# Kernel optimization log

Hardware: AMD Instinct MI355X
Metric: run time of the kernel (lower is better)

## Reference

```python
import jax, jax.numpy as jnp
import numpy as np
from jax.scipy.ndimage import map_coordinates

GRID_SIZE = 8
SIGMA = 0.05


def setup_inputs() -> dict:
    key = jax.random.key(0)
    k1, k2 = jax.random.split(key)
    B, C, D, H, W = 4, 2, 160, 160, 160
    x = jax.random.normal(k1, (B, C, D, H, W), dtype=jnp.float32)
    # torch.randn(B,3,g,g,g)*sigma hoisted out of forward for determinism
    flow_coarse = jax.random.normal(k2, (B, 3, GRID_SIZE, GRID_SIZE, GRID_SIZE), dtype=jnp.float32) * SIGMA
    return {"x": x, "flow_coarse": flow_coarse}


def _upsample_trilinear(f, D, H, W):
    # f: [g,g,g] coarse flow channel -> [D,H,W]; matches
    # F.interpolate(mode='trilinear', align_corners=True):
    # src coordinate = dst * (g-1)/(size-1), linear interp.
    g = f.shape[0]
    cz = jnp.arange(D, dtype=jnp.float32) * (g - 1) / (D - 1)
    cy = jnp.arange(H, dtype=jnp.float32) * (g - 1) / (H - 1)
    cx = jnp.arange(W, dtype=jnp.float32) * (g - 1) / (W - 1)
    mz, my, mx = jnp.meshgrid(cz, cy, cx, indexing='ij')
    return map_coordinates(f, [mz, my, mx], order=1, mode='nearest')


def reference(x, flow_coarse):
    B, C, D, H, W = x.shape
    # upsample coarse flow per (batch, channel): [B,3,D,H,W]
    up = jax.vmap(jax.vmap(lambda f: _upsample_trilinear(f, D, H, W)))(flow_coarse)
    # base normalized grid, channels ordered (x=w, y=h, z=d) as in grid_sample
    d = jnp.linspace(-1.0, 1.0, D, dtype=jnp.float32)
    h = jnp.linspace(-1.0, 1.0, H, dtype=jnp.float32)
    w = jnp.linspace(-1.0, 1.0, W, dtype=jnp.float32)
    gd, gh, gw = jnp.meshgrid(d, h, w, indexing='ij')
    gx = gw[None] + up[:, 0]  # [B,D,H,W]
    gy = gh[None] + up[:, 1]
    gz = gd[None] + up[:, 2]
    # unnormalize (align_corners=True): [-1,1] -> [0, size-1]
    ix = (gx + 1.0) * (W - 1) * 0.5
    iy = (gy + 1.0) * (H - 1) * 0.5
    iz = (gz + 1.0) * (D - 1) * 0.5

    # grid_sample 3D, bilinear(=trilinear), padding_mode='reflection',
    # align_corners=True == map_coordinates mode='mirror' (period 2*(n-1))
    def warp_bc(vol, cz, cy, cx):
        return map_coordinates(vol, [cz, cy, cx], order=1, mode='mirror')

    warp_b = jax.vmap(warp_bc, in_axes=(0, None, None, None))  # over C
    out = jax.vmap(warp_b)(x, iz, iy, ix)  # over B -> [B,C,D,H,W]
    return out
```

## Files before the change

### kernel.cpp

```cpp
#include <hip/hip_runtime.h>

#define NB 4
#define NC 2
#define ND 160
#define NH 160
#define NW 160
#define NG 8
#define HWSZ (NH * NW)
#define DHW (ND * HWSZ)
#define NTHR 256
#define NBLOCKS (NB * DHW / NTHR)
#define BLK_PER_B (DHW / NTHR)
#define BLK_PER_D (HWSZ / NTHR)
#define TILES_X 10
#define TILES_PER_SLICE 400

typedef float v2f __attribute__((ext_vector_type(2), aligned(4)));

__device__ __forceinline__ float reflect_mirror(float t) {
    t = fabsf(t);
    return fminf(t, 318.0f - t);
}

__device__ __forceinline__ float lerp_v(v2f q, float g) {
    return q.x + (q.y - q.x) * g;
}

__global__ __launch_bounds__(256) void elastic_deform_kernel(
    const float* __restrict__ x,
    const float* __restrict__ flow,
    float* __restrict__ out)
{
    int bid = blockIdx.x;
    int eff = (bid & 7) * (NBLOCKS / 8) + (bid >> 3);

    int b  = eff / BLK_PER_B;
    int e2 = eff - b * BLK_PER_B;
    int d  = e2 / BLK_PER_D;
    int e3 = e2 - d * BLK_PER_D;

    int wid  = (int)threadIdx.x >> 6;
    int lane = (int)threadIdx.x & 63;
    int tslice = e3 * 4 + wid;
    int ty = tslice / TILES_X;
    int tx = tslice - ty * TILES_X;
    int h  = ty * 4 + (lane >> 4);
    int w  = tx * 16 + (lane & 15);

    const float s = 7.0f / 159.0f;

    float cz  = (float)d * s;
    int   izb = min((int)cz, NG - 2);
    float fz  = cz - (float)izb;

    __shared__ float sfz[3 * 64];
    if (threadIdx.x < 192) {
        int ch = (int)threadIdx.x >> 6;
        int yx = (int)threadIdx.x & 63;
        const float* fp = flow + ((b * 3 + ch) * NG + izb) * 64 + yx;
        float f0 = fp[0], f1 = fp[64];
        sfz[ch * 64 + yx] = f0 + (f1 - f0) * fz;
    }
    __syncthreads();

    float cy = (float)h * s;
    float cx = (float)w * s;
    int iyb = min((int)cy, NG - 2); float fy = cy - (float)iyb;
    int ixb = min((int)cx, NG - 2); float fx = cx - (float)ixb;
    int cpos = iyb * NG + ixb;

    float u[3];
#pragma unroll
    for (int ch = 0; ch < 3; ++ch) {
        const float* p = sfz + ch * 64 + cpos;
        float f00 = p[0], f01 = p[1], f10 = p[8], f11 = p[9];
        float a0 = f00 + (f01 - f00) * fx;
        float a1 = f10 + (f11 - f10) * fx;
        u[ch] = a0 + (a1 - a0) * fy;
    }

    float sx = reflect_mirror((float)w + u[0] * 79.5f);
    float sy = reflect_mirror((float)h + u[1] * 79.5f);
    float sz = reflect_mirror((float)d + u[2] * 79.5f);

    int xb = min((int)sx, NW - 2); float gx = sx - (float)xb;
    int yb = min((int)sy, NH - 2); float gy = sy - (float)yb;
    int zb = min((int)sz, ND - 2); float gz = sz - (float)zb;

    int off = (zb * NH + yb) * NW + xb;
    const float* p0 = x + (size_t)b * (NC * DHW) + off;
    const float* p1 = p0 + DHW;

    float r0, r1;
    {
        float v00 = lerp_v(*(const v2f*)(p0), gx);
        float v01 = lerp_v(*(const v2f*)(p0 + NW), gx);
        float v10 = lerp_v(*(const v2f*)(p0 + HWSZ), gx);
        float v11 = lerp_v(*(const v2f*)(p0 + HWSZ + NW), gx);
        float a0 = v00 + (v01 - v00) * gy;
        float a1 = v10 + (v11 - v10) * gy;
        r0 = a0 + (a1 - a0) * gz;
    }
    {
        float v00 = lerp_v(*(const v2f*)(p1), gx);
        float v01 = lerp_v(*(const v2f*)(p1 + NW), gx);
        float v10 = lerp_v(*(const v2f*)(p1 + HWSZ), gx);
        float v11 = lerp_v(*(const v2f*)(p1 + HWSZ + NW), gx);
        float a0 = v00 + (v01 - v00) * gy;
        float a1 = v10 + (v11 - v10) * gy;
        r1 = a0 + (a1 - a0) * gz;
    }

    size_t opos = (size_t)b * (NC * DHW) + (size_t)(d * NH + h) * NW + w;
    __builtin_nontemporal_store(r0, out + opos);
    __builtin_nontemporal_store(r1, out + opos + DHW);
}

extern "C" void kernel_launch(void* const* d_in, const int* in_sizes, int n_in,
                              void* d_out, int out_size, void* d_ws, size_t ws_size,
                              hipStream_t stream) {
    const float* x    = (const float*)d_in[0];
    const float* flow = (const float*)d_in[1];
    float* out = (float*)d_out;
    elastic_deform_kernel<<<NBLOCKS, NTHR, 0, stream>>>(x, flow, out);
}
```

Baseline: 342.4 us.

## Compute two adjacent x outputs per thread with shared 4-wide gathers

Each thread now produces two neighbouring w outputs, loading one 4-float window per row that covers both samples and evaluating the x interpolation as a piecewise-linear blend. When the second sample lands in a different row or slice or outside the window, it falls back to separate 2-float loads. Coarse flow values are shared between the two outputs, and the stores become 2-wide. This halves the thread count and reduces the number of gather instructions, at the cost of more arithmetic, more registers and a divergent fallback path.

Measured after the change: 364.7 us. 1.06x slower.

```diff
diff --git a/kernel.cpp b/kernel.cpp
--- a/kernel.cpp
+++ b/kernel.cpp
@@ -9,21 +9,22 @@
 #define HWSZ (NH * NW)
 #define DHW (ND * HWSZ)
 #define NTHR 256
-#define NBLOCKS (NB * DHW / NTHR)
-#define BLK_PER_B (DHW / NTHR)
-#define BLK_PER_D (HWSZ / NTHR)
-#define TILES_X 10
-#define TILES_PER_SLICE 400
+#define NBLOCKS 32000
+#define BLK_PER_B 8000
+#define BLK_PER_D 50
+#define TILES_X 5
 
 typedef float v2f __attribute__((ext_vector_type(2), aligned(4)));
+typedef float v4fa __attribute__((ext_vector_type(4), aligned(4)));
 
 __device__ __forceinline__ float reflect_mirror(float t) {
     t = fabsf(t);
     return fminf(t, 318.0f - t);
 }
 
-__device__ __forceinline__ float lerp_v(v2f q, float g) {
-    return q.x + (q.y - q.x) * g;
+__device__ __forceinline__ float lerp2(const float* __restrict__ p, float g) {
+    float a = p[0], b = p[1];
+    return a + (b - a) * g;
 }
 
 __global__ __launch_bounds__(256) void elastic_deform_kernel(
@@ -45,7 +46,7 @@
     int ty = tslice / TILES_X;
     int tx = tslice - ty * TILES_X;
     int h  = ty * 4 + (lane >> 4);
-    int w  = tx * 16 + (lane & 15);
+    int w0 = tx * 32 + (lane & 15) * 2;
 
     const float s = 7.0f / 159.0f;
 
@@ -64,56 +65,122 @@
     __syncthreads();
 
     float cy = (float)h * s;
-    float cx = (float)w * s;
     int iyb = min((int)cy, NG - 2); float fy = cy - (float)iyb;
-    int ixb = min((int)cx, NG - 2); float fx = cx - (float)ixb;
-    int cpos = iyb * NG + ixb;
-
-    float u[3];
+    float cx0 = (float)w0 * s;
+    int ixa = min((int)cx0, NG - 2);
+    float e[3][3];
 #pragma unroll
     for (int ch = 0; ch < 3; ++ch) {
-        const float* p = sfz + ch * 64 + cpos;
-        float f00 = p[0], f01 = p[1], f10 = p[8], f11 = p[9];
-        float a0 = f00 + (f01 - f00) * fx;
-        float a1 = f10 + (f11 - f10) * fx;
-        u[ch] = a0 + (a1 - a0) * fy;
+        const float* p = sfz + ch * 64 + iyb * NG;
+#pragma unroll
+        for (int j = 0; j < 3; ++j) {
+            int ix = (j == 2) ? min(ixa + 2, NG - 1) : (ixa + j);
+            float f0 = p[ix], f1 = p[NG + ix];
+            e[ch][j] = f0 + (f1 - f0) * fy;
+        }
     }
 
-    float sx = reflect_mirror((float)w + u[0] * 79.5f);
-    float sy = reflect_mirror((float)h + u[1] * 79.5f);
-    float sz = reflect_mirror((float)d + u[2] * 79.5f);
+    int xb[2], yb[2], zb[2];
+    float sxv[2], gy[2], gz[2];
+#pragma unroll
+    for (int i = 0; i < 2; ++i) {
+        float cx = cx0 + (float)i * s;
+        int ixb = min((int)cx, NG - 2);
+        int oi  = ixb - ixa;
+        float fx = cx - (float)ixb;
+        float s0, s1;
+        s0 = oi ? e[0][1] : e[0][0];  s1 = oi ? e[0][2] : e[0][1];
+        float ux = s0 + (s1 - s0) * fx;
+        s0 = oi ? e[1][1] : e[1][0];  s1 = oi ? e[1][2] : e[1][1];
+        float uy = s0 + (s1 - s0) * fx;
+        s0 = oi ? e[2][1] : e[2][0];  s1 = oi ? e[2][2] : e[2][1];
+        float uz = s0 + (s1 - s0) * fx;
 
-    int xb = min((int)sx, NW - 2); float gx = sx - (float)xb;
-    int yb = min((int)sy, NH - 2); float gy = sy - (float)yb;
-    int zb = min((int)sz, ND - 2); float gz = sz - (float)zb;
+        float sx = reflect_mirror((float)(w0 + i) + ux * 79.5f);
+        float sy = reflect_mirror((float)h + uy * 79.5f);
+        float sz = reflect_mirror((float)d + uz * 79.5f);
+        xb[i] = min((int)sx, NW - 2); sxv[i] = sx;
+        yb[i] = min((int)sy, NH - 2); gy[i] = sy - (float)yb[i];
+        zb[i] = min((int)sz, ND - 2); gz[i] = sz - (float)zb[i];
+    }
 
-    int off = (zb * NH + yb) * NW + xb;
-    const float* p0 = x + (size_t)b * (NC * DHW) + off;
+    int xq = min(xb[0], NW - 4);
+    const float* basep = x + (size_t)b * (NC * DHW);
+    const float* p0 = basep + (zb[0] * NH + yb[0]) * NW + xq;
     const float* p1 = p0 + DHW;
 
-    float r0, r1;
+    v4fa qa0 = *(const v4fa*)(p0);
+    v4fa qa1 = *(const v4fa*)(p0 + NW);
+    v4fa qa2 = *(const v4fa*)(p0 + HWSZ);
+    v4fa qa3 = *(const v4fa*)(p0 + HWSZ + NW);
+    v4fa qb0 = *(const v4fa*)(p1);
+    v4fa qb1 = *(const v4fa*)(p1 + NW);
+    v4fa qb2 = *(const v4fa*)(p1 + HWSZ);
+    v4fa qb3 = *(const v4fa*)(p1 + HWSZ + NW);
+
+    float posA = sxv[0] - (float)xq;
+    float A1 = fminf(posA, 1.0f);
+    float A2 = fminf(fmaxf(posA - 1.0f, 0.0f), 1.0f);
+    float A3 = fminf(fmaxf(posA - 2.0f, 0.0f), 1.0f);
+    float posB = sxv[1] - (float)xq;
+    float B1 = fminf(posB, 1.0f);
+    float B2 = fminf(fmaxf(posB - 1.0f, 0.0f), 1.0f);
+    float B3 = fminf(fmaxf(posB - 2.0f, 0.0f), 1.0f);
+
+#define PWL(q, m1, m2, m3) \
+    ((q).x + (m1) * ((q).y - (q).x) + (m2) * ((q).z - (q).y) + (m3) * ((q).w - (q).z))
+
+    float r0c0, r0c1;
     {
-        float v00 = lerp_v(*(const v2f*)(p0), gx);
-        float v01 = lerp_v(*(const v2f*)(p0 + NW), gx);
-        float v10 = lerp_v(*(const v2f*)(p0 + HWSZ), gx);
-        float v11 = lerp_v(*(const v2f*)(p0 + HWSZ + NW), gx);
-        float a0 = v00 + (v01 - v00) * gy;
-        float a1 = v10 + (v11 - v10) * gy;
-        r0 = a0 + (a1 - a0) * gz;
-    }
-    {
-        float v00 = lerp_v(*(const v2f*)(p1), gx);
-        float v01 = lerp_v(*(const v2f*)(p1 + NW), gx);
-        float v10 = lerp_v(*(const v2f*)(p1 + HWSZ), gx);
-        float v11 = lerp_v(*(const v2f*)(p1 + HWSZ + NW), gx);
-        float a0 = v00 + (v01 - v00) * gy;
-        float a1 = v10 + (v11 - v10) * gy;
-        r1 = a0 + (a1 - a0) * gz;
+        float a0 = PWL(qa0, A1, A2, A3) + (PWL(qa1, A1, A2, A3) - PWL(qa0, A1, A2, A3)) * gy[0];
+        float a1 = PWL(qa2, A1, A2, A3) + (PWL(qa3, A1, A2, A3) - PWL(qa2, A1, A2, A3)) * gy[0];
+        r0c0 = a0 + (a1 - a0) * gz[0];
+        float b0 = PWL(qb0, A1, A2, A3) + (PWL(qb1, A1, A2, A3) - PWL(qb0, A1, A2, A3)) * gy[0];
+        float b1 = PWL(qb2, A1, A2, A3) + (PWL(qb3, A1, A2, A3) - PWL(qb2, A1, A2, A3)) * gy[0];
+        r0c1 = b0 + (b1 - b0) * gz[0];
     }
 
-    size_t opos = (size_t)b * (NC * DHW) + (size_t)(d * NH + h) * NW + w;
-    __builtin_nontemporal_store(r0, out + opos);
-    __builtin_nontemporal_store(r1, out + opos + DHW);
+    float r1c0, r1c1;
+    {
+        float a0 = PWL(qa0, B1, B2, B3) + (PWL(qa1, B1, B2, B3) - PWL(qa0, B1, B2, B3)) * gy[1];
+        float a1 = PWL(qa2, B1, B2, B3) + (PWL(qa3, B1, B2, B3) - PWL(qa2, B1, B2, B3)) * gy[1];
+        r1c0 = a0 + (a1 - a0) * gz[1];
+        float b0 = PWL(qb0, B1, B2, B3) + (PWL(qb1, B1, B2, B3) - PWL(qb0, B1, B2, B3)) * gy[1];
+        float b1 = PWL(qb2, B1, B2, B3) + (PWL(qb3, B1, B2, B3) - PWL(qb2, B1, B2, B3)) * gy[1];
+        r1c1 = b0 + (b1 - b0) * gz[1];
+    }
+
+    bool rep = (zb[1] != zb[0]) | (yb[1] != yb[0]) |
+               ((unsigned)(xb[1] - xq) > 2u);
+    if (rep) {
+        float gx1 = sxv[1] - (float)xb[1];
+        const float* t0 = basep + (zb[1] * NH + yb[1]) * NW + xb[1];
+        const float* t1 = t0 + DHW;
+        {
+            float v00 = lerp2(t0, gx1);
+            float v01 = lerp2(t0 + NW, gx1);
+            float v10 = lerp2(t0 + HWSZ, gx1);
+            float v11 = lerp2(t0 + HWSZ + NW, gx1);
+            float a0 = v00 + (v01 - v00) * gy[1];
+            float a1 = v10 + (v11 - v10) * gy[1];
+            r1c0 = a0 + (a1 - a0) * gz[1];
+        }
+        {
+            float v00 = lerp2(t1, gx1);
+            float v01 = lerp2(t1 + NW, gx1);
+            float v10 = lerp2(t1 + HWSZ, gx1);
+            float v11 = lerp2(t1 + HWSZ + NW, gx1);
+            float a0 = v00 + (v01 - v00) * gy[1];
+            float a1 = v10 + (v11 - v10) * gy[1];
+            r1c1 = a0 + (a1 - a0) * gz[1];
+        }
+    }
+
+    size_t opos = (size_t)b * (NC * DHW) + (size_t)(d * NH + h) * NW + w0;
+    v2f o0 = { r0c0, r1c0 };
+    v2f o1 = { r0c1, r1c1 };
+    __builtin_nontemporal_store(o0, (v2f*)(out + opos));
+    __builtin_nontemporal_store(o1, (v2f*)(out + opos + DHW));
 }
 
 extern "C" void kernel_launch(void* const* d_in, const int* in_sizes, int n_in,
```
